# Kernel optimization log

Hardware: AMD Instinct MI355X
Metric: run time of the kernel (lower is better)

## Reference

```python
import jax, jax.numpy as jnp
import numpy as np

ALPHA = 0.99
EPS = 1e-14


def setup_inputs() -> dict:
    key = jax.random.key(0)
    B, C, T, F = 16, 1, 2000, 481
    x = jax.random.normal(key, (B, C, T, F, 2), dtype=jnp.float32)
    # unit_norm_init: linearly decaying initial norm state over freq bins
    init_state = jnp.linspace(0.001, 0.0001, F, dtype=jnp.float32).reshape(1, 1, F, 1)
    return {"x": x, "init_state": init_state}


def reference(x, init_state):
    # x: [B, C, T, F, 2] (real/imag), init_state: [1, 1, F, 1]
    B, C, T, F, _ = x.shape
    # complex magnitude per (b,c,t,f), clamped for stability: [B, C, T, F, 1]
    x_abs = jnp.sqrt(jnp.maximum(jnp.sum(x * x, axis=-1, keepdims=True), EPS))
    # scan over time: state = (1-alpha)*|x_t| + alpha*state
    xs = jnp.moveaxis(x_abs, 2, 0)  # [T, B, C, F, 1]
    s0 = jnp.broadcast_to(init_state, (B, C, F, 1)).astype(x.dtype)

    def step(s, xt):
        s = xt * (1.0 - ALPHA) + s * ALPHA
        return s, s

    _, states = jax.lax.scan(step, s0, xs)  # [T, B, C, F, 1]
    states = jnp.moveaxis(states, 0, 2)  # [B, C, T, F, 1]
    return x / jnp.sqrt(states)
```

## Files before the change

kernel.cpp:

```cpp
#include <hip/hip_runtime.h>


#define ALPHA_F 0.99f
#define OMA_F   0.01f

constexpr int Bn = 16;
constexpr int Tn = 2000;
constexpr int Fn = 481;
constexpr int NC = 50;
constexpr int L  = Tn / NC;
constexpr int UN = 10;
#define ALPHA_L 0.668971758f

__global__ __launch_bounds__(256) void eun_pass1(
    const float* __restrict__ x, float* __restrict__ part) {
  const int f = blockIdx.x * blockDim.x + threadIdx.x;
  if (f >= Fn) return;
  const int b = blockIdx.y;
  const int c = blockIdx.z;

  const size_t stride = (size_t)Fn * 2;
  const float* xp = x + ((size_t)b * Tn + (size_t)c * L) * stride + (size_t)f * 2;

  float s = 0.f;
  for (int t0 = 0; t0 < L; t0 += UN) {
    float2 v[UN];
#pragma unroll
    for (int j = 0; j < UN; ++j)
      v[j] = *(const float2*)(xp + (size_t)j * stride);
#pragma unroll
    for (int j = 0; j < UN; ++j) {
      float m = sqrtf(fmaxf(v[j].x * v[j].x + v[j].y * v[j].y, 1e-14f));
      s = fmaf(ALPHA_F, s, OMA_F * m);
    }
    xp += (size_t)UN * stride;
  }
  part[((size_t)b * NC + c) * Fn + f] = s;
}

__global__ __launch_bounds__(256) void eun_mid(
    const float* __restrict__ part, const float* __restrict__ init_state,
    float* __restrict__ start) {
  const int f = blockIdx.x * blockDim.x + threadIdx.x;
  if (f >= Fn) return;
  const int b = blockIdx.y;

  const float* pp = part + (size_t)b * NC * Fn + f;
  float p[NC];
#pragma unroll
  for (int c = 0; c < NC; ++c) p[c] = pp[(size_t)c * Fn];

  float s = init_state[f];
  float* sp = start + (size_t)b * NC * Fn + f;
#pragma unroll
  for (int c = 0; c < NC; ++c) {
    sp[(size_t)c * Fn] = s;
    s = fmaf(s, ALPHA_L, p[c]);
  }
}

__global__ __launch_bounds__(256) void eun_pass2(
    const float* __restrict__ x, const float* __restrict__ start,
    float* __restrict__ out) {
  const int f = blockIdx.x * blockDim.x + threadIdx.x;
  if (f >= Fn) return;
  const int b = blockIdx.y;
  const int c = blockIdx.z;

  float s = start[((size_t)b * NC + c) * Fn + f];

  const size_t stride = (size_t)Fn * 2;
  const size_t off = ((size_t)b * Tn + (size_t)c * L) * stride + (size_t)f * 2;
  const float* xp = x + off;
  float*       op = out + off;

  for (int t0 = 0; t0 < L; t0 += UN) {
    float2 v[UN];
#pragma unroll
    for (int j = 0; j < UN; ++j)
      v[j] = *(const float2*)(xp + (size_t)j * stride);
#pragma unroll
    for (int j = 0; j < UN; ++j) {
      float m = sqrtf(fmaxf(v[j].x * v[j].x + v[j].y * v[j].y, 1e-14f));
      s = fmaf(ALPHA_F, s, OMA_F * m);
      float inv = rsqrtf(s);
      union { float2 f2; unsigned long long u; } cvt;
      cvt.f2 = make_float2(v[j].x * inv, v[j].y * inv);
      __builtin_nontemporal_store(cvt.u,
          (unsigned long long*)(op + (size_t)j * stride));
    }
    xp += (size_t)UN * stride;
    op += (size_t)UN * stride;
  }
}

extern "C" void kernel_launch(void* const* d_in, const int* in_sizes, int n_in,
                              void* d_out, int out_size, void* d_ws, size_t ws_size,
                              hipStream_t stream) {
  const float* x    = (const float*)d_in[0];
  const float* init = (const float*)d_in[1];
  float* out        = (float*)d_out;
  float* part       = (float*)d_ws;
  float* start      = (float*)d_ws + (size_t)Bn * NC * Fn;

  dim3 grid3((Fn + 255) / 256, Bn, NC);
  eun_pass1<<<grid3, dim3(256), 0, stream>>>(x, part);
  eun_mid<<<dim3((Fn + 255) / 256, Bn), dim3(256), 0, stream>>>(part, init, start);
  eun_pass2<<<grid3, dim3(256), 0, stream>>>(x, start, out);
}
```

Measured before the change: 242.7 us.

## Fuse three-pass chunked scan into single kernel with decoupled look-back

Merges the chunk-partial, carry-propagation and normalization kernels into one kernel. Each chunk block publishes its partial sum to workspace (pre-filled with NaN via memset) and spins on predecessors' partials to build its starting state, then re-reads its chunk to write outputs. This removes two kernel launches and the separate mid pass, and improves cache locality for the second read of x. It risks spin-wait stalls and relies on earlier chunks being scheduled first.

```diff
diff --git a/kernel.cpp b/kernel.cpp
--- a/kernel.cpp
+++ b/kernel.cpp
@@ -3,6 +3,7 @@
 
 #define ALPHA_F 0.99f
 #define OMA_F   0.01f
+#define EPS_F   1e-14f
 
 constexpr int Bn = 16;
 constexpr int Tn = 2000;
@@ -12,17 +13,19 @@
 constexpr int UN = 10;
 #define ALPHA_L 0.668971758f
 
-__global__ __launch_bounds__(256) void eun_pass1(
-    const float* __restrict__ x, float* __restrict__ part) {
+__global__ __launch_bounds__(256) void eun_fused(
+    const float* __restrict__ x, const float* __restrict__ init_state,
+    float* __restrict__ out, float* __restrict__ part) {
   const int f = blockIdx.x * blockDim.x + threadIdx.x;
   if (f >= Fn) return;
   const int b = blockIdx.y;
   const int c = blockIdx.z;
 
   const size_t stride = (size_t)Fn * 2;
-  const float* xp = x + ((size_t)b * Tn + (size_t)c * L) * stride + (size_t)f * 2;
+  const size_t off = ((size_t)b * Tn + (size_t)c * L) * stride + (size_t)f * 2;
 
-  float s = 0.f;
+  const float* xp = x + off;
+  float p = 0.f;
   for (int t0 = 0; t0 < L; t0 += UN) {
     float2 v[UN];
 #pragma unroll
@@ -30,50 +33,32 @@
       v[j] = *(const float2*)(xp + (size_t)j * stride);
 #pragma unroll
     for (int j = 0; j < UN; ++j) {
-      float m = sqrtf(fmaxf(v[j].x * v[j].x + v[j].y * v[j].y, 1e-14f));
-      s = fmaf(ALPHA_F, s, OMA_F * m);
+      float m = sqrtf(fmaxf(fmaf(v[j].x, v[j].x, v[j].y * v[j].y), EPS_F));
+      p = fmaf(ALPHA_F, p, OMA_F * m);
     }
     xp += (size_t)UN * stride;
   }
-  part[((size_t)b * NC + c) * Fn + f] = s;
-}
 
-__global__ __launch_bounds__(256) void eun_mid(
-    const float* __restrict__ part, const float* __restrict__ init_state,
-    float* __restrict__ start) {
-  const int f = blockIdx.x * blockDim.x + threadIdx.x;
-  if (f >= Fn) return;
-  const int b = blockIdx.y;
+  float* pb = part + (size_t)b * NC * Fn + f;
+  __hip_atomic_store(pb + (size_t)c * Fn, p,
+                     __ATOMIC_RELAXED, __HIP_MEMORY_SCOPE_AGENT);
 
-  const float* pp = part + (size_t)b * NC * Fn + f;
-  float p[NC];
-#pragma unroll
-  for (int c = 0; c < NC; ++c) p[c] = pp[(size_t)c * Fn];
+  float acc = 0.f, w = 1.f;
+  for (int j = c - 1; j >= 0; --j) {
+    float pv = __hip_atomic_load(pb + (size_t)j * Fn,
+                                 __ATOMIC_RELAXED, __HIP_MEMORY_SCOPE_AGENT);
+    while (!(pv > 0.f)) {
+      __builtin_amdgcn_s_sleep(1);
+      pv = __hip_atomic_load(pb + (size_t)j * Fn,
+                             __ATOMIC_RELAXED, __HIP_MEMORY_SCOPE_AGENT);
+    }
+    acc = fmaf(w, pv, acc);
+    w *= ALPHA_L;
+  }
+  float s = fmaf(w, init_state[f], acc);
 
-  float s = init_state[f];
-  float* sp = start + (size_t)b * NC * Fn + f;
-#pragma unroll
-  for (int c = 0; c < NC; ++c) {
-    sp[(size_t)c * Fn] = s;
-    s = fmaf(s, ALPHA_L, p[c]);
-  }
-}
-
-__global__ __launch_bounds__(256) void eun_pass2(
-    const float* __restrict__ x, const float* __restrict__ start,
-    float* __restrict__ out) {
-  const int f = blockIdx.x * blockDim.x + threadIdx.x;
-  if (f >= Fn) return;
-  const int b = blockIdx.y;
-  const int c = blockIdx.z;
-
-  float s = start[((size_t)b * NC + c) * Fn + f];
-
-  const size_t stride = (size_t)Fn * 2;
-  const size_t off = ((size_t)b * Tn + (size_t)c * L) * stride + (size_t)f * 2;
-  const float* xp = x + off;
-  float*       op = out + off;
-
+  xp = x + off;
+  float* op = out + off;
   for (int t0 = 0; t0 < L; t0 += UN) {
     float2 v[UN];
 #pragma unroll
@@ -81,7 +66,7 @@
       v[j] = *(const float2*)(xp + (size_t)j * stride);
 #pragma unroll
     for (int j = 0; j < UN; ++j) {
-      float m = sqrtf(fmaxf(v[j].x * v[j].x + v[j].y * v[j].y, 1e-14f));
+      float m = sqrtf(fmaxf(fmaf(v[j].x, v[j].x, v[j].y * v[j].y), EPS_F));
       s = fmaf(ALPHA_F, s, OMA_F * m);
       float inv = rsqrtf(s);
       union { float2 f2; unsigned long long u; } cvt;
@@ -101,10 +86,9 @@
   const float* init = (const float*)d_in[1];
   float* out        = (float*)d_out;
   float* part       = (float*)d_ws;
-  float* start      = (float*)d_ws + (size_t)Bn * NC * Fn;
 
-  dim3 grid3((Fn + 255) / 256, Bn, NC);
-  eun_pass1<<<grid3, dim3(256), 0, stream>>>(x, part);
-  eun_mid<<<dim3((Fn + 255) / 256, Bn), dim3(256), 0, stream>>>(part, init, start);
-  eun_pass2<<<grid3, dim3(256), 0, stream>>>(x, start, out);
+  hipMemsetAsync(part, 0xFF, (size_t)Bn * NC * Fn * sizeof(float), stream);
+
+  dim3 grid((Fn + 255) / 256, Bn, NC);
+  eun_fused<<<grid, dim3(256), 0, stream>>>(x, init, out, part);
 }
```

Result: slower. 249.0 us (+2.6%).

## Fuse chunk-prefix scan into pass2 with truncated geometric window

Applied to the files above, without the earlier changes.

Removes the separate serial mid kernel. Each pass2 thread now rebuilds its chunk's starting state from up to W=24 preceding chunk partials, weighted by powers of ALPHA_L, and adds the init state only when the window reaches the start. This saves one launch and the serial 50-step dependency, at the cost of redundant partial loads per thread and a truncation error of about ALPHA_L^24 for later chunks. It also swaps the nontemporal stores for plain stores and uses an fma for the magnitude.

```diff
diff --git a/kernel.cpp b/kernel.cpp
--- a/kernel.cpp
+++ b/kernel.cpp
@@ -3,6 +3,7 @@
 
 #define ALPHA_F 0.99f
 #define OMA_F   0.01f
+#define EPS_F   1e-14f
 
 constexpr int Bn = 16;
 constexpr int Tn = 2000;
@@ -10,6 +11,7 @@
 constexpr int NC = 50;
 constexpr int L  = Tn / NC;
 constexpr int UN = 10;
+constexpr int W  = 24;
 #define ALPHA_L 0.668971758f
 
 __global__ __launch_bounds__(256) void eun_pass1(
@@ -30,7 +32,7 @@
       v[j] = *(const float2*)(xp + (size_t)j * stride);
 #pragma unroll
     for (int j = 0; j < UN; ++j) {
-      float m = sqrtf(fmaxf(v[j].x * v[j].x + v[j].y * v[j].y, 1e-14f));
+      float m = sqrtf(fmaxf(fmaf(v[j].x, v[j].x, v[j].y * v[j].y), EPS_F));
       s = fmaf(ALPHA_F, s, OMA_F * m);
     }
     xp += (size_t)UN * stride;
@@ -38,36 +40,25 @@
   part[((size_t)b * NC + c) * Fn + f] = s;
 }
 
-__global__ __launch_bounds__(256) void eun_mid(
-    const float* __restrict__ part, const float* __restrict__ init_state,
-    float* __restrict__ start) {
-  const int f = blockIdx.x * blockDim.x + threadIdx.x;
-  if (f >= Fn) return;
-  const int b = blockIdx.y;
-
-  const float* pp = part + (size_t)b * NC * Fn + f;
-  float p[NC];
-#pragma unroll
-  for (int c = 0; c < NC; ++c) p[c] = pp[(size_t)c * Fn];
-
-  float s = init_state[f];
-  float* sp = start + (size_t)b * NC * Fn + f;
-#pragma unroll
-  for (int c = 0; c < NC; ++c) {
-    sp[(size_t)c * Fn] = s;
-    s = fmaf(s, ALPHA_L, p[c]);
-  }
-}
-
 __global__ __launch_bounds__(256) void eun_pass2(
-    const float* __restrict__ x, const float* __restrict__ start,
-    float* __restrict__ out) {
+    const float* __restrict__ x, const float* __restrict__ part,
+    const float* __restrict__ init_state, float* __restrict__ out) {
   const int f = blockIdx.x * blockDim.x + threadIdx.x;
   if (f >= Fn) return;
   const int b = blockIdx.y;
   const int c = blockIdx.z;
 
-  float s = start[((size_t)b * NC + c) * Fn + f];
+  const float* pb = part + (size_t)b * NC * Fn + f;
+  const int n = (c < W) ? c : W;
+  float pv[W];
+#pragma unroll
+  for (int k = 0; k < W; ++k)
+    if (k < n) pv[k] = pb[(size_t)(c - 1 - k) * Fn];
+  float s = 0.f, w = 1.f;
+#pragma unroll
+  for (int k = 0; k < W; ++k)
+    if (k < n) { s = fmaf(w, pv[k], s); w *= ALPHA_L; }
+  if (c <= W) s = fmaf(w, init_state[f], s);
 
   const size_t stride = (size_t)Fn * 2;
   const size_t off = ((size_t)b * Tn + (size_t)c * L) * stride + (size_t)f * 2;
@@ -81,13 +72,10 @@
       v[j] = *(const float2*)(xp + (size_t)j * stride);
 #pragma unroll
     for (int j = 0; j < UN; ++j) {
-      float m = sqrtf(fmaxf(v[j].x * v[j].x + v[j].y * v[j].y, 1e-14f));
+      float m = sqrtf(fmaxf(fmaf(v[j].x, v[j].x, v[j].y * v[j].y), EPS_F));
       s = fmaf(ALPHA_F, s, OMA_F * m);
       float inv = rsqrtf(s);
-      union { float2 f2; unsigned long long u; } cvt;
-      cvt.f2 = make_float2(v[j].x * inv, v[j].y * inv);
-      __builtin_nontemporal_store(cvt.u,
-          (unsigned long long*)(op + (size_t)j * stride));
+      *(float2*)(op + (size_t)j * stride) = make_float2(v[j].x * inv, v[j].y * inv);
     }
     xp += (size_t)UN * stride;
     op += (size_t)UN * stride;
@@ -101,10 +89,8 @@
   const float* init = (const float*)d_in[1];
   float* out        = (float*)d_out;
   float* part       = (float*)d_ws;
-  float* start      = (float*)d_ws + (size_t)Bn * NC * Fn;
 
-  dim3 grid3((Fn + 255) / 256, Bn, NC);
-  eun_pass1<<<grid3, dim3(256), 0, stream>>>(x, part);
-  eun_mid<<<dim3((Fn + 255) / 256, Bn), dim3(256), 0, stream>>>(part, init, start);
-  eun_pass2<<<grid3, dim3(256), 0, stream>>>(x, start, out);
+  dim3 grid((Fn + 255) / 256, Bn, NC);
+  eun_pass1<<<grid, dim3(256), 0, stream>>>(x, part);
+  eun_pass2<<<grid, dim3(256), 0, stream>>>(x, part, init, out);
 }
```

Result: slower. 255.5 us (+5.3%).
